# Kernel tuning notes

Measured on AMD Instinct MI355X. Metric: run time of the kernel, lower is better.

## Reference

```python
import jax, jax.numpy as jnp
import numpy as np


def setup_inputs() -> dict:
    key = jax.random.key(0)
    ks = jax.random.split(key, 7)
    B, S, H, I, E = 2, 512, 2048, 4096, 8
    W = 0.02  # init scale for weights
    return {
        "hidden_states": jax.random.normal(ks[0], (B, S, H), jnp.float32),
        "router_w": jax.random.normal(ks[1], (H, E), jnp.float32) * W,
        "gate_up_proj": jax.random.normal(ks[2], (E, H, 2 * I), jnp.float32) * W,
        "down_proj": jax.random.normal(ks[3], (E, I, H), jnp.float32) * W,
        "shared_gate_w": jax.random.normal(ks[4], (H, I), jnp.float32) * W,
        "shared_up_w": jax.random.normal(ks[5], (H, I), jnp.float32) * W,
        "shared_down_w": jax.random.normal(ks[6], (I, H), jnp.float32) * W,
        "top_k": 1,
    }


def reference(hidden_states, router_w, gate_up_proj, down_proj,
              shared_gate_w, shared_up_w, shared_down_w, top_k):
    H = hidden_states.shape[-1]
    x = hidden_states.reshape(-1, H)                      # [T, H]
    T = x.shape[0]

    # Router: top-k logits scattered into -inf, then sigmoid -> sparse scores
    router_logits = x @ router_w                          # [T, E]
    top_val, top_idx = jax.lax.top_k(router_logits, top_k)
    scores = jnp.full_like(router_logits, -jnp.inf)
    scores = scores.at[jnp.arange(T)[:, None], top_idx].set(top_val)
    router_scores = jax.nn.sigmoid(scores.astype(jnp.float32)).astype(x.dtype).T  # [E, T]

    # Dense 'repeat all experts' dispatch (as in the original module)
    routed_in = x[None, :, :] * router_scores[:, :, None]  # [E, T, H]
    gate_up = jnp.einsum('eth,ehf->etf', routed_in, gate_up_proj)  # [E, T, 2I]
    gate, up = jnp.split(gate_up, 2, axis=-1)
    routed_out = jnp.einsum('eti,eih->eth', up * jax.nn.silu(gate), down_proj)  # [E, T, H]

    # Shared expert MLP (SwiGLU)
    shared = (jax.nn.silu(x @ shared_gate_w) * (x @ shared_up_w)) @ shared_down_w  # [T, H]

    out = shared + routed_out.sum(axis=0)                 # [T, H]
    return out, router_scores
```

## Files before the change

### kernel.cpp

```cpp
#include <hip/hip_runtime.h>
#include <hip/hip_bf16.h>

#define H_DIM 2048
#define I_DIM 4096
#define NE 8
#define NT 1024

#define BM 128
#define BN 64
#define BK 32

typedef __bf16 bf16x8 __attribute__((ext_vector_type(8)));
typedef float f32x4 __attribute__((ext_vector_type(4)));
typedef unsigned short u16x8 __attribute__((ext_vector_type(8)));

__device__ __forceinline__ unsigned short f2bf(float f) {
  return __builtin_bit_cast(unsigned short, (__bf16)f);
}

__device__ __forceinline__ void gl2lds16(const void* g, void* l) {
  __builtin_amdgcn_global_load_lds(
      (const __attribute__((address_space(1))) unsigned int*)g,
      (__attribute__((address_space(3))) unsigned int*)l, 16, 0, 0);
}

#define VMCNT0() asm volatile("s_waitcnt vmcnt(0)" ::: "memory")

__global__ __launch_bounds__(256) void router_kernel(
    const float* __restrict__ x, const float* __restrict__ rw,
    float* __restrict__ rs_out, int* __restrict__ expert_of,
    float* __restrict__ score_of, int* __restrict__ counts)
{
  const int lane = threadIdx.x & 63;
  const int wv = threadIdx.x >> 6;
  const int t = blockIdx.x * 4 + wv;
  float acc[NE];
#pragma unroll
  for (int e = 0; e < NE; ++e) acc[e] = 0.f;
  const float* xr = x + (size_t)t * H_DIM;
  for (int h0 = 0; h0 < H_DIM; h0 += 64) {
    const float xv = xr[h0 + lane];
    const float* rwp = rw + (size_t)(h0 + lane) * NE;
    const f32x4 r0 = *(const f32x4*)rwp;
    const f32x4 r1 = *(const f32x4*)(rwp + 4);
#pragma unroll
    for (int e = 0; e < 4; ++e) { acc[e] += xv * r0[e]; acc[e + 4] += xv * r1[e]; }
  }
#pragma unroll
  for (int e = 0; e < NE; ++e) {
    acc[e] += __shfl_xor(acc[e], 32, 64);
    acc[e] += __shfl_xor(acc[e], 16, 64);
    acc[e] += __shfl_xor(acc[e], 8, 64);
    acc[e] += __shfl_xor(acc[e], 4, 64);
    acc[e] += __shfl_xor(acc[e], 2, 64);
    acc[e] += __shfl_xor(acc[e], 1, 64);
  }
  int best = 0; float bv = acc[0];
#pragma unroll
  for (int e = 1; e < NE; ++e) if (acc[e] > bv) { bv = acc[e]; best = e; }
  const float score = 1.f / (1.f + __expf(-bv));
  if (lane < NE) rs_out[(size_t)lane * NT + t] = (lane == best) ? score : 0.f;
  if (lane == 0) {
    expert_of[t] = best;
    score_of[t] = score;
    atomicAdd(&counts[best], 1);
  }
}

__global__ void offsets_kernel(const int* __restrict__ counts,
                               int* __restrict__ offsets, int* __restrict__ cursor)
{
  if (threadIdx.x == 0) {
    int run = 0;
#pragma unroll
    for (int e = 0; e < NE; ++e) { offsets[e] = run; run += counts[e]; cursor[e] = 0; }
  }
}

__global__ void scatter_kernel(const int* __restrict__ expert_of,
                               const int* __restrict__ offsets,
                               int* __restrict__ cursor, int* __restrict__ perm)
{
  const int t = blockIdx.x * 256 + threadIdx.x;
  const int e = expert_of[t];
  const int p = atomicAdd(&cursor[e], 1);
  perm[offsets[e] + p] = t;
}

__global__ __launch_bounds__(256) void gather_kernel(
    const float* __restrict__ x, const int* __restrict__ perm,
    const float* __restrict__ score_of, unsigned short* __restrict__ xb,
    unsigned short* __restrict__ xs)
{
  const int b = blockIdx.x;
  const int c = threadIdx.x * 8;
  const int src = perm[b];
  const float s = score_of[src];
  const float* xrow = x + (size_t)b * H_DIM + c;
  const float* srow = x + (size_t)src * H_DIM + c;
  u16x8 vb, vs;
#pragma unroll
  for (int j = 0; j < 8; ++j) {
    vb[j] = f2bf(xrow[j]);
    vs[j] = f2bf(srow[j] * s);
  }
  *(u16x8*)&xb[(size_t)b * H_DIM + c] = vb;
  *(u16x8*)&xs[(size_t)b * H_DIM + c] = vs;
}

__global__ __launch_bounds__(256) void gemm1_kernel(
    const unsigned short* __restrict__ xs, const unsigned short* __restrict__ xb,
    const float* __restrict__ gup, const float* __restrict__ sgw,
    const float* __restrict__ suw, unsigned short* __restrict__ act_r,
    unsigned short* __restrict__ act_s, const int* __restrict__ counts,
    const int* __restrict__ offsets)
{
  const int e = blockIdx.z;
  int cnt, roff; size_t ldw;
  const unsigned short* X; const float* Wg; const float* Wu; unsigned short* OUT;
  if (e < NE) {
    cnt = counts[e]; roff = offsets[e]; ldw = 2 * I_DIM;
    X = xs; Wg = gup + (size_t)e * H_DIM * 2 * I_DIM; Wu = Wg + I_DIM; OUT = act_r;
  } else {
    cnt = NT; roff = 0; ldw = I_DIM;
    X = xb; Wg = sgw; Wu = suw; OUT = act_s;
  }
  const int m0 = blockIdx.x * BM;
  if (m0 >= cnt) return;
  const int n0 = blockIdx.y * BN;

  __shared__ char lds[49152];
  char* const xl  = lds;
  char* const wgl = lds + 16384;
  char* const wul = lds + 32768;

  const int tid = threadIdx.x, lane = tid & 63, w = tid >> 6;

  const char* sp[6]; size_t inc[6]; char* dstb[6];
#pragma unroll
  for (int s = 0; s < 6; ++s) {
    const int g = w * 6 + s;
    if (g < 8) {
      const int m = 16 * g + (lane >> 2);
      const int c = lane & 3;
      const int msrc = (m0 + m < cnt) ? (roff + m0 + m) : roff;
      sp[s] = (const char*)(X + (size_t)msrc * H_DIM + ((c ^ ((m >> 1) & 3)) << 3));
      inc[s] = (size_t)BK * 2;
      dstb[s] = xl + g * 1024;
    } else {
      const int ks = (g - 8) & 7;
      const int r = 4 * ks + (lane >> 4);
      const int cs = (lane & 15) ^ (((r >> 3) & 3) << 1);
      const float* Wb = (g < 16) ? Wg : Wu;
      sp[s] = (const char*)(Wb + (size_t)r * ldw + n0 + (cs << 2));
      inc[s] = (size_t)BK * ldw * 4;
      dstb[s] = ((g < 16) ? wgl : wul) + ks * 1024;
    }
  }

#define STAGE1(CUR) do {                                                 \
  _Pragma("unroll")                                                      \
  for (int s = 0; s < 6; ++s) {                                          \
    gl2lds16(sp[s], dstb[s] + (CUR) * 8192);                             \
    sp[s] += inc[s];                                                     \
  }                                                                      \
} while (0)

  const int q = lane >> 4, l15 = lane & 15;
  const int nl = w * 16 + l15;
  const int wro = q * 2048 + ((nl << 2) ^ (q << 5));
  const int xro = l15 * 64 + ((q ^ ((l15 >> 1) & 3)) << 4);

  f32x4 accg[8] = {};
  f32x4 accu[8] = {};

#define COMPUTE1(CUR) do {                                               \
  const char* _xb = xl + (CUR) * 8192 + xro;                             \
  const char* _wg = wgl + (CUR) * 8192 + wro;                            \
  const char* _wu = wul + (CUR) * 8192 + wro;                            \
  float _g32[8], _u32[8];                                                \
  _Pragma("unroll")                                                      \
  for (int j = 0; j < 8; ++j) {                                          \
    _g32[j] = *(const float*)(_wg + j * 256);                            \
    _u32[j] = *(const float*)(_wu + j * 256);                            \
  }                                                                      \
  bf16x8 _gf, _uf;                                                       \
  _Pragma("unroll")                                                      \
  for (int j = 0; j < 8; ++j) { _gf[j] = (__bf16)_g32[j];                \
                                _uf[j] = (__bf16)_u32[j]; }              \
  _Pragma("unroll")                                                      \
  for (int mb = 0; mb < 8; ++mb) {                                       \
    const u16x8 _xr = *(const u16x8*)(_xb + mb * 1024);                  \
    const bf16x8 _xf = __builtin_bit_cast(bf16x8, _xr);                  \
    accg[mb] = __builtin_amdgcn_mfma_f32_16x16x32_bf16(_gf, _xf, accg[mb], 0, 0, 0); \
    accu[mb] = __builtin_amdgcn_mfma_f32_16x16x32_bf16(_uf, _xf, accu[mb], 0, 0, 0); \
  }                                                                      \
} while (0)

  STAGE1(0);
  VMCNT0();
  __syncthreads();
  int cur = 0;
  for (int t = 0; t < H_DIM / BK - 1; ++t) {
    STAGE1(cur ^ 1);
    COMPUTE1(cur);
    VMCNT0();
    __syncthreads();
    cur ^= 1;
  }
  COMPUTE1(cur);

  const int nw = n0 + w * 16 + (q * 4);
#pragma unroll
  for (int mb = 0; mb < 8; ++mb) {
    const int m = m0 + mb * 16 + l15;
    if (m < cnt) {
      unsigned short o[4];
#pragma unroll
      for (int r = 0; r < 4; ++r) {
        const float g = accg[mb][r];
        const float u = accu[mb][r];
        const float sg = g / (1.f + __expf(-g));
        o[r] = f2bf(sg * u);
      }
      uint2 pk;
      pk.x = (unsigned)o[0] | ((unsigned)o[1] << 16);
      pk.y = (unsigned)o[2] | ((unsigned)o[3] << 16);
      *(uint2*)&OUT[(size_t)(roff + m) * I_DIM + nw] = pk;
    }
  }
}

__global__ __launch_bounds__(256) void gemm2_kernel(
    const unsigned short* __restrict__ ACT, const float* __restrict__ wd_base,
    float* __restrict__ OUT, const int* __restrict__ counts,
    const int* __restrict__ offsets, const int* __restrict__ perm,
    const int accumulate)
{
  const int e = blockIdx.z;
  const int cnt = counts ? counts[e] : NT;
  const int roff = offsets ? offsets[e] : 0;
  const int m0 = blockIdx.x * BM;
  if (m0 >= cnt) return;
  const int n0 = blockIdx.y * BN;
  const float* Wd = wd_base + (size_t)e * I_DIM * H_DIM;

  __shared__ char lds[32768];
  char* const xl  = lds;
  char* const wdl = lds + 16384;

  const int tid = threadIdx.x, lane = tid & 63, w = tid >> 6;

  const char* sp[4]; size_t inc[4]; char* dstb[4];
#pragma unroll
  for (int s = 0; s < 4; ++s) {
    const int g = w * 4 + s;
    if (g < 8) {
      const int m = 16 * g + (lane >> 2);
      const int c = lane & 3;
      const int msrc = (m0 + m < cnt) ? (roff + m0 + m) : roff;
      sp[s] = (const char*)(ACT + (size_t)msrc * I_DIM + ((c ^ ((m >> 1) & 3)) << 3));
      inc[s] = (size_t)BK * 2;
      dstb[s] = xl + g * 1024;
    } else {
      const int ks = (g - 8) & 7;
      const int r = 4 * ks + (lane >> 4);
      const int cs = (lane & 15) ^ (((r >> 3) & 3) << 1);
      sp[s] = (const char*)(Wd + (size_t)r * H_DIM + n0 + (cs << 2));
      inc[s] = (size_t)BK * H_DIM * 4;
      dstb[s] = wdl + ks * 1024;
    }
  }

#define STAGE2(CUR) do {                                                 \
  _Pragma("unroll")                                                      \
  for (int s = 0; s < 4; ++s) {                                          \
    gl2lds16(sp[s], dstb[s] + (CUR) * 8192);                             \
    sp[s] += inc[s];                                                     \
  }                                                                      \
} while (0)

  const int q = lane >> 4, l15 = lane & 15;
  const int nl = w * 16 + l15;
  const int wro = q * 2048 + ((nl << 2) ^ (q << 5));
  const int xro = l15 * 64 + ((q ^ ((l15 >> 1) & 3)) << 4);

  f32x4 acc[8] = {};

#define COMPUTE2(CUR) do {                                               \
  const char* _xb = xl + (CUR) * 8192 + xro;                             \
  const char* _wd = wdl + (CUR) * 8192 + wro;                            \
  float _d32[8];                                                         \
  _Pragma("unroll")                                                      \
  for (int j = 0; j < 8; ++j) _d32[j] = *(const float*)(_wd + j * 256);  \
  bf16x8 _df;                                                            \
  _Pragma("unroll")                                                      \
  for (int j = 0; j < 8; ++j) _df[j] = (__bf16)_d32[j];                  \
  _Pragma("unroll")                                                      \
  for (int mb = 0; mb < 8; ++mb) {                                       \
    const u16x8 _xr = *(const u16x8*)(_xb + mb * 1024);                  \
    const bf16x8 _xf = __builtin_bit_cast(bf16x8, _xr);                  \
    acc[mb] = __builtin_amdgcn_mfma_f32_16x16x32_bf16(_df, _xf, acc[mb], 0, 0, 0); \
  }                                                                      \
} while (0)

  STAGE2(0);
  VMCNT0();
  __syncthreads();
  int cur = 0;
  for (int t = 0; t < I_DIM / BK - 1; ++t) {
    STAGE2(cur ^ 1);
    COMPUTE2(cur);
    VMCNT0();
    __syncthreads();
    cur ^= 1;
  }
  COMPUTE2(cur);

  const int nw = n0 + w * 16 + (q * 4);
#pragma unroll
  for (int mb = 0; mb < 8; ++mb) {
    const int m = m0 + mb * 16 + l15;
    if (m < cnt) {
      const int t = perm ? perm[roff + m] : m;
      float* orow = OUT + (size_t)t * H_DIM + nw;
      f32x4 v = acc[mb];
      if (accumulate) {
        const f32x4 old = *(const f32x4*)orow;
        v += old;
      }
      *(f32x4*)orow = v;
    }
  }
}

extern "C" void kernel_launch(void* const* d_in, const int* in_sizes, int n_in,
                              void* d_out, int out_size, void* d_ws, size_t ws_size,
                              hipStream_t stream)
{
  const float* x   = (const float*)d_in[0];
  const float* rw  = (const float*)d_in[1];
  const float* gup = (const float*)d_in[2];
  const float* dwn = (const float*)d_in[3];
  const float* sgw = (const float*)d_in[4];
  const float* suw = (const float*)d_in[5];
  const float* sdw = (const float*)d_in[6];
  float* out = (float*)d_out;
  float* rs_out = out + (size_t)NT * H_DIM;

  char* ws = (char*)d_ws;
  int* counts   = (int*)ws;
  int* cursor   = (int*)(ws + 32);
  int* offsets  = (int*)(ws + 64);
  int* expert_of = (int*)(ws + 128);
  float* score_of = (float*)(ws + 128 + 4096);
  int* perm     = (int*)(ws + 128 + 8192);
  unsigned short* xb    = (unsigned short*)(ws + 16384);
  unsigned short* xs    = xb + (size_t)NT * H_DIM;
  unsigned short* act_s = xs + (size_t)NT * H_DIM;
  unsigned short* act_r = act_s + (size_t)NT * I_DIM;

  hipMemsetAsync(counts, 0, 64, stream);
  router_kernel<<<dim3(NT / 4), dim3(256), 0, stream>>>(x, rw, rs_out, expert_of, score_of, counts);
  offsets_kernel<<<dim3(1), dim3(64), 0, stream>>>(counts, offsets, cursor);
  scatter_kernel<<<dim3(NT / 256), dim3(256), 0, stream>>>(expert_of, offsets, cursor, perm);
  gather_kernel<<<dim3(NT), dim3(256), 0, stream>>>(x, perm, score_of, xb, xs);
  gemm1_kernel<<<dim3(NT / BM, I_DIM / BN, NE + 1), dim3(256), 0, stream>>>(
      xs, xb, gup, sgw, suw, act_r, act_s, counts, offsets);
  gemm2_kernel<<<dim3(NT / BM, H_DIM / BN, 1), dim3(256), 0, stream>>>(
      act_s, sdw, out, nullptr, nullptr, nullptr, 0);
  gemm2_kernel<<<dim3(NT / BM, H_DIM / BN, NE), dim3(256), 0, stream>>>(
      act_r, dwn, out, counts, offsets, perm, 1);
}
```

Before: 1.152 ms.

## Deepen GEMM pipelines with partial vmcnt waits and 4-stage weight buffering

Both expert GEMM kernels now wait only for the oldest stage's global-to-LDS loads (partial vmcnt) instead of draining all loads before each barrier, so prefetches overlap compute. The down-projection kernel gets a four-deep weight ring buffer with LDS grown to 48KB and a two-deep activation buffer, and the weight-stage assignment is split evenly across waves. LDS weight read offsets are changed to match the new staging layout. Larger LDS may reduce occupancy, and the vmcnt counts must match the per-thread issue counts exactly for correctness.

```diff
diff --git a/kernel.cpp b/kernel.cpp
--- a/kernel.cpp
+++ b/kernel.cpp
@@ -10,6 +10,9 @@
 #define BN 64
 #define BK 32
 
+#define NSTEP1 (H_DIM / BK)
+#define NSTEP2 (I_DIM / BK)
+
 typedef __bf16 bf16x8 __attribute__((ext_vector_type(8)));
 typedef float f32x4 __attribute__((ext_vector_type(4)));
 typedef unsigned short u16x8 __attribute__((ext_vector_type(8)));
@@ -24,7 +27,8 @@
       (__attribute__((address_space(3))) unsigned int*)l, 16, 0, 0);
 }
 
-#define VMCNT0() asm volatile("s_waitcnt vmcnt(0)" ::: "memory")
+#define FENCE() asm volatile("" ::: "memory")
+#define BAR() __builtin_amdgcn_s_barrier()
 
 __global__ __launch_bounds__(256) void router_kernel(
     const float* __restrict__ x, const float* __restrict__ rw,
@@ -181,8 +185,8 @@
   float _g32[8], _u32[8];                                                \
   _Pragma("unroll")                                                      \
   for (int j = 0; j < 8; ++j) {                                          \
-    _g32[j] = *(const float*)(_wg + j * 256);                            \
-    _u32[j] = *(const float*)(_wu + j * 256);                            \
+    _g32[j] = *(const float*)(_wg + (j >> 2) * 1024 + (j & 3) * 256);    \
+    _u32[j] = *(const float*)(_wu + (j >> 2) * 1024 + (j & 3) * 256);    \
   }                                                                      \
   bf16x8 _gf, _uf;                                                       \
   _Pragma("unroll")                                                      \
@@ -198,17 +202,19 @@
 } while (0)
 
   STAGE1(0);
-  VMCNT0();
-  __syncthreads();
-  int cur = 0;
-  for (int t = 0; t < H_DIM / BK - 1; ++t) {
-    STAGE1(cur ^ 1);
-    COMPUTE1(cur);
-    VMCNT0();
-    __syncthreads();
-    cur ^= 1;
-  }
-  COMPUTE1(cur);
+  for (int t = 0; t < NSTEP1 - 1; ++t) {
+    STAGE1((t + 1) & 1);
+    asm volatile("s_waitcnt vmcnt(6)" ::: "memory");
+    BAR();
+    FENCE();
+    COMPUTE1(t & 1);
+    FENCE();
+    BAR();
+  }
+  asm volatile("s_waitcnt vmcnt(0)" ::: "memory");
+  BAR();
+  FENCE();
+  COMPUTE1((NSTEP1 - 1) & 1);
 
   const int nw = n0 + w * 16 + (q * 4);
 #pragma unroll
@@ -245,38 +251,48 @@
   const int n0 = blockIdx.y * BN;
   const float* Wd = wd_base + (size_t)e * I_DIM * H_DIM;
 
-  __shared__ char lds[32768];
+  __shared__ char lds[49152];
   char* const xl  = lds;
   char* const wdl = lds + 16384;
 
   const int tid = threadIdx.x, lane = tid & 63, w = tid >> 6;
 
-  const char* sp[4]; size_t inc[4]; char* dstb[4];
-#pragma unroll
-  for (int s = 0; s < 4; ++s) {
-    const int g = w * 4 + s;
-    if (g < 8) {
+  const char* spx[2]; char* dstx[2];
+  const char* spw[2]; char* dstw[2];
+#pragma unroll
+  for (int s = 0; s < 2; ++s) {
+    {
+      const int g = w * 2 + s;
       const int m = 16 * g + (lane >> 2);
       const int c = lane & 3;
       const int msrc = (m0 + m < cnt) ? (roff + m0 + m) : roff;
-      sp[s] = (const char*)(ACT + (size_t)msrc * I_DIM + ((c ^ ((m >> 1) & 3)) << 3));
-      inc[s] = (size_t)BK * 2;
-      dstb[s] = xl + g * 1024;
-    } else {
-      const int ks = (g - 8) & 7;
+      spx[s] = (const char*)(ACT + (size_t)msrc * I_DIM + ((c ^ ((m >> 1) & 3)) << 3));
+      dstx[s] = xl + g * 1024;
+    }
+    {
+      const int ks = w * 2 + s;
       const int r = 4 * ks + (lane >> 4);
       const int cs = (lane & 15) ^ (((r >> 3) & 3) << 1);
-      sp[s] = (const char*)(Wd + (size_t)r * H_DIM + n0 + (cs << 2));
-      inc[s] = (size_t)BK * H_DIM * 4;
-      dstb[s] = wdl + ks * 1024;
+      spw[s] = (const char*)(Wd + (size_t)r * H_DIM + n0 + (cs << 2));
+      dstw[s] = wdl + ks * 1024;
     }
   }
-
-#define STAGE2(CUR) do {                                                 \
-  _Pragma("unroll")                                                      \
-  for (int s = 0; s < 4; ++s) {                                          \
-    gl2lds16(sp[s], dstb[s] + (CUR) * 8192);                             \
-    sp[s] += inc[s];                                                     \
+  const size_t incx = (size_t)BK * 2;
+  const size_t incw = (size_t)BK * H_DIM * 4;
+
+#define STAGEX2(CUR) do {                                                \
+  _Pragma("unroll")                                                      \
+  for (int s = 0; s < 2; ++s) {                                          \
+    gl2lds16(spx[s], dstx[s] + (CUR) * 8192);                            \
+    spx[s] += incx;                                                      \
+  }                                                                      \
+} while (0)
+
+#define STAGEW2(CUR) do {                                                \
+  _Pragma("unroll")                                                      \
+  for (int s = 0; s < 2; ++s) {                                          \
+    gl2lds16(spw[s], dstw[s] + (CUR) * 8192);                            \
+    spw[s] += incw;                                                      \
   }                                                                      \
 } while (0)
 
@@ -287,12 +303,13 @@
 
   f32x4 acc[8] = {};
 
-#define COMPUTE2(CUR) do {                                               \
-  const char* _xb = xl + (CUR) * 8192 + xro;                             \
-  const char* _wd = wdl + (CUR) * 8192 + wro;                            \
+#define COMPUTE2(BX, BW) do {                                            \
+  const char* _xb = xl + (BX) * 8192 + xro;                              \
+  const char* _wd = wdl + (BW) * 8192 + wro;                             \
   float _d32[8];                                                         \
   _Pragma("unroll")                                                      \
-  for (int j = 0; j < 8; ++j) _d32[j] = *(const float*)(_wd + j * 256);  \
+  for (int j = 0; j < 8; ++j)                                            \
+    _d32[j] = *(const float*)(_wd + (j >> 2) * 1024 + (j & 3) * 256);    \
   bf16x8 _df;                                                            \
   _Pragma("unroll")                                                      \
   for (int j = 0; j < 8; ++j) _df[j] = (__bf16)_d32[j];                  \
@@ -304,18 +321,30 @@
   }                                                                      \
 } while (0)
 
-  STAGE2(0);
-  VMCNT0();
-  __syncthreads();
-  int cur = 0;
-  for (int t = 0; t < I_DIM / BK - 1; ++t) {
-    STAGE2(cur ^ 1);
-    COMPUTE2(cur);
-    VMCNT0();
-    __syncthreads();
-    cur ^= 1;
-  }
-  COMPUTE2(cur);
+  STAGEX2(0);
+  STAGEW2(0);
+  STAGEW2(1);
+  for (int t = 0; t < NSTEP2 - 2; ++t) {
+    STAGEX2((t + 1) & 1);
+    STAGEW2((t + 2) & 3);
+    asm volatile("s_waitcnt vmcnt(6)" ::: "memory");
+    BAR();
+    FENCE();
+    COMPUTE2(t & 1, t & 3);
+    FENCE();
+    BAR();
+  }
+  STAGEX2((NSTEP2 - 1) & 1);
+  asm volatile("s_waitcnt vmcnt(4)" ::: "memory");
+  BAR();
+  FENCE();
+  COMPUTE2((NSTEP2 - 2) & 1, (NSTEP2 - 2) & 3);
+  FENCE();
+  BAR();
+  asm volatile("s_waitcnt vmcnt(0)" ::: "memory");
+  BAR();
+  FENCE();
+  COMPUTE2((NSTEP2 - 1) & 1, (NSTEP2 - 1) & 3);
 
   const int nw = n0 + w * 16 + (q * 4);
 #pragma unroll
```

Result: faster. 1.103 ms, median of 5 (-4.2%).

## Pre-convert weights to bf16 and triple-buffer GEMM pipelines with staggered K start

Applied to the files above, without the earlier changes.

Adds a conversion pass that writes all expert and shared weights as bf16 into workspace on every call. The GEMMs then stream half-width weights and skip the per-tile fp32-to-bf16 conversion. Both GEMMs move from double to triple buffering with partial vmcnt waits, and each block starts its K loop at a different offset to spread memory traffic. The conversion pass itself reads all fp32 weights once and writes the bf16 copies, roughly 1.5x the weight bytes the GEMMs used to stream. It is likely a net loss, because in the old code most blocks find few or no routed tokens and each weight tile is read only a handful of times.

```diff
diff --git a/kernel.cpp b/kernel.cpp
--- a/kernel.cpp
+++ b/kernel.cpp
@@ -9,6 +9,8 @@
 #define BM 128
 #define BN 64
 #define BK 32
+#define NS1 (H_DIM / BK)
+#define NS2 (I_DIM / BK)
 
 typedef __bf16 bf16x8 __attribute__((ext_vector_type(8)));
 typedef float f32x4 __attribute__((ext_vector_type(4)));
@@ -24,7 +26,24 @@
       (__attribute__((address_space(3))) unsigned int*)l, 16, 0, 0);
 }
 
-#define VMCNT0() asm volatile("s_waitcnt vmcnt(0)" ::: "memory")
+#define FENCE() asm volatile("" ::: "memory")
+#define BAR() __builtin_amdgcn_s_barrier()
+#define VMC(N) asm volatile("s_waitcnt vmcnt(" #N ")" ::: "memory")
+
+__global__ __launch_bounds__(256) void convert_kernel(
+    const float* __restrict__ src, unsigned short* __restrict__ dst, int n8)
+{
+  int i = blockIdx.x * 256 + threadIdx.x;
+  const int stride = gridDim.x * 256;
+  for (; i < n8; i += stride) {
+    const f32x4 a = ((const f32x4*)src)[2 * (size_t)i];
+    const f32x4 b = ((const f32x4*)src)[2 * (size_t)i + 1];
+    u16x8 o;
+#pragma unroll
+    for (int j = 0; j < 4; ++j) { o[j] = f2bf(a[j]); o[4 + j] = f2bf(b[j]); }
+    ((u16x8*)dst)[i] = o;
+  }
+}
 
 __global__ __launch_bounds__(256) void router_kernel(
     const float* __restrict__ x, const float* __restrict__ rw,
@@ -110,20 +129,21 @@
 
 __global__ __launch_bounds__(256) void gemm1_kernel(
     const unsigned short* __restrict__ xs, const unsigned short* __restrict__ xb,
-    const float* __restrict__ gup, const float* __restrict__ sgw,
-    const float* __restrict__ suw, unsigned short* __restrict__ act_r,
+    const unsigned short* __restrict__ gupb, const unsigned short* __restrict__ sgwb,
+    const unsigned short* __restrict__ suwb, unsigned short* __restrict__ act_r,
     unsigned short* __restrict__ act_s, const int* __restrict__ counts,
     const int* __restrict__ offsets)
 {
   const int e = blockIdx.z;
   int cnt, roff; size_t ldw;
-  const unsigned short* X; const float* Wg; const float* Wu; unsigned short* OUT;
+  const unsigned short* X; const unsigned short* Wg; const unsigned short* Wu;
+  unsigned short* OUT;
   if (e < NE) {
     cnt = counts[e]; roff = offsets[e]; ldw = 2 * I_DIM;
-    X = xs; Wg = gup + (size_t)e * H_DIM * 2 * I_DIM; Wu = Wg + I_DIM; OUT = act_r;
+    X = xs; Wg = gupb + (size_t)e * H_DIM * 2 * I_DIM; Wu = Wg + I_DIM; OUT = act_r;
   } else {
     cnt = NT; roff = 0; ldw = I_DIM;
-    X = xb; Wg = sgw; Wu = suw; OUT = act_s;
+    X = xb; Wg = sgwb; Wu = suwb; OUT = act_s;
   }
   const int m0 = blockIdx.x * BM;
   if (m0 >= cnt) return;
@@ -131,63 +151,55 @@
 
   __shared__ char lds[49152];
   char* const xl  = lds;
-  char* const wgl = lds + 16384;
-  char* const wul = lds + 32768;
-
-  const int tid = threadIdx.x, lane = tid & 63, w = tid >> 6;
-
-  const char* sp[6]; size_t inc[6]; char* dstb[6];
-#pragma unroll
-  for (int s = 0; s < 6; ++s) {
-    const int g = w * 6 + s;
-    if (g < 8) {
-      const int m = 16 * g + (lane >> 2);
-      const int c = lane & 3;
-      const int msrc = (m0 + m < cnt) ? (roff + m0 + m) : roff;
-      sp[s] = (const char*)(X + (size_t)msrc * H_DIM + ((c ^ ((m >> 1) & 3)) << 3));
-      inc[s] = (size_t)BK * 2;
-      dstb[s] = xl + g * 1024;
-    } else {
-      const int ks = (g - 8) & 7;
-      const int r = 4 * ks + (lane >> 4);
-      const int cs = (lane & 15) ^ (((r >> 3) & 3) << 1);
-      const float* Wb = (g < 16) ? Wg : Wu;
-      sp[s] = (const char*)(Wb + (size_t)r * ldw + n0 + (cs << 2));
-      inc[s] = (size_t)BK * ldw * 4;
-      dstb[s] = ((g < 16) ? wgl : wul) + ks * 1024;
-    }
-  }
-
-#define STAGE1(CUR) do {                                                 \
-  _Pragma("unroll")                                                      \
-  for (int s = 0; s < 6; ++s) {                                          \
-    gl2lds16(sp[s], dstb[s] + (CUR) * 8192);                             \
-    sp[s] += inc[s];                                                     \
-  }                                                                      \
+  char* const wgl = lds + 24576;
+  char* const wul = lds + 36864;
+
+  const int lane = threadIdx.x & 63, w = threadIdx.x >> 6;
+
+  const unsigned short* spx[2]; int dx[2];
+#pragma unroll
+  for (int s = 0; s < 2; ++s) {
+    const int g = w * 2 + s;
+    const int m = 16 * g + (lane >> 2);
+    const int c = lane & 3;
+    const int msrc = (m0 + m < cnt) ? (roff + m0 + m) : roff;
+    spx[s] = X + (size_t)msrc * H_DIM + ((c ^ ((m >> 1) & 3)) << 3);
+    dx[s] = g * 1024;
+  }
+  const int wr = 8 * w + (lane >> 3);
+  const int wc = (lane & 7) ^ ((w & 3) << 1);
+  const unsigned short* spg = Wg + (size_t)wr * ldw + n0 + (wc << 3);
+  const unsigned short* spu = Wu + (size_t)wr * ldw + n0 + (wc << 3);
+  const int dw = w * 1024;
+
+#define STAGE1(BUF, POS) do {                                            \
+  const size_t _xo = (size_t)(POS) * BK;                                 \
+  const size_t _wo = (size_t)(POS) * BK * ldw;                           \
+  gl2lds16(spx[0] + _xo, xl + (BUF) * 8192 + dx[0]);                     \
+  gl2lds16(spx[1] + _xo, xl + (BUF) * 8192 + dx[1]);                     \
+  gl2lds16(spg + _wo, wgl + (BUF) * 4096 + dw);                          \
+  gl2lds16(spu + _wo, wul + (BUF) * 4096 + dw);                          \
 } while (0)
 
   const int q = lane >> 4, l15 = lane & 15;
-  const int nl = w * 16 + l15;
-  const int wro = q * 2048 + ((nl << 2) ^ (q << 5));
   const int xro = l15 * 64 + ((q ^ ((l15 >> 1) & 3)) << 4);
+  const int wbase = (q * 8) * 128 + (((w * 16 + l15) * 2) ^ (q << 5));
 
   f32x4 accg[8] = {};
   f32x4 accu[8] = {};
 
-#define COMPUTE1(CUR) do {                                               \
-  const char* _xb = xl + (CUR) * 8192 + xro;                             \
-  const char* _wg = wgl + (CUR) * 8192 + wro;                            \
-  const char* _wu = wul + (CUR) * 8192 + wro;                            \
-  float _g32[8], _u32[8];                                                \
+#define COMP1(BUF) do {                                                  \
+  const char* _xb = xl + (BUF) * 8192 + xro;                             \
+  const char* _wg = wgl + (BUF) * 4096 + wbase;                          \
+  const char* _wu = wul + (BUF) * 4096 + wbase;                          \
+  u16x8 _gb, _ub;                                                        \
   _Pragma("unroll")                                                      \
   for (int j = 0; j < 8; ++j) {                                          \
-    _g32[j] = *(const float*)(_wg + j * 256);                            \
-    _u32[j] = *(const float*)(_wu + j * 256);                            \
+    _gb[j] = *(const unsigned short*)(_wg + j * 128);                    \
+    _ub[j] = *(const unsigned short*)(_wu + j * 128);                    \
   }                                                                      \
-  bf16x8 _gf, _uf;                                                       \
-  _Pragma("unroll")                                                      \
-  for (int j = 0; j < 8; ++j) { _gf[j] = (__bf16)_g32[j];                \
-                                _uf[j] = (__bf16)_u32[j]; }              \
+  const bf16x8 _gf = __builtin_bit_cast(bf16x8, _gb);                    \
+  const bf16x8 _uf = __builtin_bit_cast(bf16x8, _ub);                    \
   _Pragma("unroll")                                                      \
   for (int mb = 0; mb < 8; ++mb) {                                       \
     const u16x8 _xr = *(const u16x8*)(_xb + mb * 1024);                  \
@@ -197,18 +209,26 @@
   }                                                                      \
 } while (0)
 
-  STAGE1(0);
-  VMCNT0();
-  __syncthreads();
-  int cur = 0;
-  for (int t = 0; t < H_DIM / BK - 1; ++t) {
-    STAGE1(cur ^ 1);
-    COMPUTE1(cur);
-    VMCNT0();
-    __syncthreads();
-    cur ^= 1;
-  }
-  COMPUTE1(cur);
+  const int k0s = (blockIdx.x * 17 + blockIdx.y * 5 + blockIdx.z * 23) & (NS1 - 1);
+  {
+    int p1 = k0s + 1; if (p1 >= NS1) p1 -= NS1;
+    STAGE1(0, k0s);
+    STAGE1(1, p1);
+  }
+  for (int t = 0; t < NS1; ++t) {
+    if (t + 2 < NS1) {
+      int p = k0s + t + 2; if (p >= NS1) p -= NS1;
+      STAGE1((t + 2) % 3, p);
+      VMC(8);
+    } else if (t + 2 == NS1) {
+      VMC(4);
+    } else {
+      VMC(0);
+    }
+    BAR(); FENCE();
+    COMP1(t % 3);
+    FENCE(); BAR();
+  }
 
   const int nw = n0 + w * 16 + (q * 4);
 #pragma unroll
@@ -232,7 +252,7 @@
 }
 
 __global__ __launch_bounds__(256) void gemm2_kernel(
-    const unsigned short* __restrict__ ACT, const float* __restrict__ wd_base,
+    const unsigned short* __restrict__ ACT, const unsigned short* __restrict__ wd_base,
     float* __restrict__ OUT, const int* __restrict__ counts,
     const int* __restrict__ offsets, const int* __restrict__ perm,
     const int accumulate)
@@ -243,59 +263,51 @@
   const int m0 = blockIdx.x * BM;
   if (m0 >= cnt) return;
   const int n0 = blockIdx.y * BN;
-  const float* Wd = wd_base + (size_t)e * I_DIM * H_DIM;
-
-  __shared__ char lds[32768];
+  const unsigned short* Wd = wd_base + (size_t)e * I_DIM * H_DIM;
+
+  __shared__ char lds[36864];
   char* const xl  = lds;
-  char* const wdl = lds + 16384;
-
-  const int tid = threadIdx.x, lane = tid & 63, w = tid >> 6;
-
-  const char* sp[4]; size_t inc[4]; char* dstb[4];
-#pragma unroll
-  for (int s = 0; s < 4; ++s) {
-    const int g = w * 4 + s;
-    if (g < 8) {
-      const int m = 16 * g + (lane >> 2);
-      const int c = lane & 3;
-      const int msrc = (m0 + m < cnt) ? (roff + m0 + m) : roff;
-      sp[s] = (const char*)(ACT + (size_t)msrc * I_DIM + ((c ^ ((m >> 1) & 3)) << 3));
-      inc[s] = (size_t)BK * 2;
-      dstb[s] = xl + g * 1024;
-    } else {
-      const int ks = (g - 8) & 7;
-      const int r = 4 * ks + (lane >> 4);
-      const int cs = (lane & 15) ^ (((r >> 3) & 3) << 1);
-      sp[s] = (const char*)(Wd + (size_t)r * H_DIM + n0 + (cs << 2));
-      inc[s] = (size_t)BK * H_DIM * 4;
-      dstb[s] = wdl + ks * 1024;
-    }
-  }
-
-#define STAGE2(CUR) do {                                                 \
+  char* const wdl = lds + 24576;
+
+  const int lane = threadIdx.x & 63, w = threadIdx.x >> 6;
+
+  const unsigned short* spx[2]; int dx[2];
+#pragma unroll
+  for (int s = 0; s < 2; ++s) {
+    const int g = w * 2 + s;
+    const int m = 16 * g + (lane >> 2);
+    const int c = lane & 3;
+    const int msrc = (m0 + m < cnt) ? (roff + m0 + m) : roff;
+    spx[s] = ACT + (size_t)msrc * I_DIM + ((c ^ ((m >> 1) & 3)) << 3);
+    dx[s] = g * 1024;
+  }
+  const int wr = 8 * w + (lane >> 3);
+  const int wc = (lane & 7) ^ ((w & 3) << 1);
+  const unsigned short* spw = Wd + (size_t)wr * H_DIM + n0 + (wc << 3);
+  const int dw = w * 1024;
+
+#define STAGE2(BUF, POS) do {                                            \
+  const size_t _xo = (size_t)(POS) * BK;                                 \
+  const size_t _wo = (size_t)(POS) * BK * H_DIM;                         \
+  gl2lds16(spx[0] + _xo, xl + (BUF) * 8192 + dx[0]);                     \
+  gl2lds16(spx[1] + _xo, xl + (BUF) * 8192 + dx[1]);                     \
+  gl2lds16(spw + _wo, wdl + (BUF) * 4096 + dw);                          \
+} while (0)
+
+  const int q = lane >> 4, l15 = lane & 15;
+  const int xro = l15 * 64 + ((q ^ ((l15 >> 1) & 3)) << 4);
+  const int wbase = (q * 8) * 128 + (((w * 16 + l15) * 2) ^ (q << 5));
+
+  f32x4 acc[8] = {};
+
+#define COMP2(BUF) do {                                                  \
+  const char* _xb = xl + (BUF) * 8192 + xro;                             \
+  const char* _wd = wdl + (BUF) * 4096 + wbase;                          \
+  u16x8 _db;                                                             \
   _Pragma("unroll")                                                      \
-  for (int s = 0; s < 4; ++s) {                                          \
-    gl2lds16(sp[s], dstb[s] + (CUR) * 8192);                             \
-    sp[s] += inc[s];                                                     \
-  }                                                                      \
-} while (0)
-
-  const int q = lane >> 4, l15 = lane & 15;
-  const int nl = w * 16 + l15;
-  const int wro = q * 2048 + ((nl << 2) ^ (q << 5));
-  const int xro = l15 * 64 + ((q ^ ((l15 >> 1) & 3)) << 4);
-
-  f32x4 acc[8] = {};
-
-#define COMPUTE2(CUR) do {                                               \
-  const char* _xb = xl + (CUR) * 8192 + xro;                             \
-  const char* _wd = wdl + (CUR) * 8192 + wro;                            \
-  float _d32[8];                                                         \
-  _Pragma("unroll")                                                      \
-  for (int j = 0; j < 8; ++j) _d32[j] = *(const float*)(_wd + j * 256);  \
-  bf16x8 _df;                                                            \
-  _Pragma("unroll")                                                      \
-  for (int j = 0; j < 8; ++j) _df[j] = (__bf16)_d32[j];                  \
+  for (int j = 0; j < 8; ++j)                                            \
+    _db[j] = *(const unsigned short*)(_wd + j * 128);                    \
+  const bf16x8 _df = __builtin_bit_cast(bf16x8, _db);                    \
   _Pragma("unroll")                                                      \
   for (int mb = 0; mb < 8; ++mb) {                                       \
     const u16x8 _xr = *(const u16x8*)(_xb + mb * 1024);                  \
@@ -304,18 +316,26 @@
   }                                                                      \
 } while (0)
 
-  STAGE2(0);
-  VMCNT0();
-  __syncthreads();
-  int cur = 0;
-  for (int t = 0; t < I_DIM / BK - 1; ++t) {
-    STAGE2(cur ^ 1);
-    COMPUTE2(cur);
-    VMCNT0();
-    __syncthreads();
-    cur ^= 1;
-  }
-  COMPUTE2(cur);
+  const int k0s = (blockIdx.x * 29 + blockIdx.y * 11 + blockIdx.z * 37) & (NS2 - 1);
+  {
+    int p1 = k0s + 1; if (p1 >= NS2) p1 -= NS2;
+    STAGE2(0, k0s);
+    STAGE2(1, p1);
+  }
+  for (int t = 0; t < NS2; ++t) {
+    if (t + 2 < NS2) {
+      int p = k0s + t + 2; if (p >= NS2) p -= NS2;
+      STAGE2((t + 2) % 3, p);
+      VMC(6);
+    } else if (t + 2 == NS2) {
+      VMC(3);
+    } else {
+      VMC(0);
+    }
+    BAR(); FENCE();
+    COMP2(t % 3);
+    FENCE(); BAR();
+  }
 
   const int nw = n0 + w * 16 + (q * 4);
 #pragma unroll
@@ -349,26 +369,42 @@
   float* rs_out = out + (size_t)NT * H_DIM;
 
   char* ws = (char*)d_ws;
-  int* counts   = (int*)ws;
-  int* cursor   = (int*)(ws + 32);
-  int* offsets  = (int*)(ws + 64);
+  int* counts    = (int*)ws;
+  int* cursor    = (int*)(ws + 32);
+  int* offsets   = (int*)(ws + 64);
   int* expert_of = (int*)(ws + 128);
   float* score_of = (float*)(ws + 128 + 4096);
-  int* perm     = (int*)(ws + 128 + 8192);
+  int* perm      = (int*)(ws + 128 + 8192);
   unsigned short* xb    = (unsigned short*)(ws + 16384);
   unsigned short* xs    = xb + (size_t)NT * H_DIM;
-  unsigned short* act_s = xs + (size_t)NT * H_DIM;
-  unsigned short* act_r = act_s + (size_t)NT * I_DIM;
+  unsigned short* act_r = xs + (size_t)NT * H_DIM;
+  unsigned short* act_s = act_r + (size_t)NT * I_DIM;
+  unsigned short* gupb  = act_s + (size_t)NT * I_DIM;
+  unsigned short* dwnb  = gupb + (size_t)NE * H_DIM * 2 * I_DIM;
+  unsigned short* sgwb  = dwnb + (size_t)NE * I_DIM * H_DIM;
+  unsigned short* suwb  = sgwb + (size_t)H_DIM * I_DIM;
+  unsigned short* sdwb  = suwb + (size_t)H_DIM * I_DIM;
+
+  const int n8_gup = NE * H_DIM * 2 * I_DIM / 8;
+  const int n8_dwn = NE * I_DIM * H_DIM / 8;
+  const int n8_sh  = H_DIM * I_DIM / 8;
 
   hipMemsetAsync(counts, 0, 64, stream);
+  convert_kernel<<<dim3(8192), dim3(256), 0, stream>>>(gup, gupb, n8_gup);
+  convert_kernel<<<dim3(8192), dim3(256), 0, stream>>>(dwn, dwnb, n8_dwn);
+  convert_kernel<<<dim3(4096), dim3(256), 0, stream>>>(sgw, sgwb, n8_sh);
+  convert_kernel<<<dim3(4096), dim3(256), 0, stream>>>(suw, suwb, n8_sh);
+  convert_kernel<<<dim3(4096), dim3(256), 0, stream>>>(sdw, sdwb, n8_sh);
+
   router_kernel<<<dim3(NT / 4), dim3(256), 0, stream>>>(x, rw, rs_out, expert_of, score_of, counts);
   offsets_kernel<<<dim3(1), dim3(64), 0, stream>>>(counts, offsets, cursor);
   scatter_kernel<<<dim3(NT / 256), dim3(256), 0, stream>>>(expert_of, offsets, cursor, perm);
   gather_kernel<<<dim3(NT), dim3(256), 0, stream>>>(x, perm, score_of, xb, xs);
+
   gemm1_kernel<<<dim3(NT / BM, I_DIM / BN, NE + 1), dim3(256), 0, stream>>>(
-      xs, xb, gup, sgw, suw, act_r, act_s, counts, offsets);
+      xs, xb, gupb, sgwb, suwb, act_r, act_s, counts, offsets);
   gemm2_kernel<<<dim3(NT / BM, H_DIM / BN, 1), dim3(256), 0, stream>>>(
-      act_s, sdw, out, nullptr, nullptr, nullptr, 0);
+      act_s, sdwb, out, nullptr, nullptr, nullptr, 0);
   gemm2_kernel<<<dim3(NT / BM, H_DIM / BN, NE), dim3(256), 0, stream>>>(
-      act_r, dwn, out, counts, offsets, perm, 1);
-}
+      act_r, dwnb, out, counts, offsets, perm, 1);
+}
```

After: 1.078 ms. -6.4%, faster.
